# Performance work log

Measured on AMD Instinct MI355X. Metric: run time of the kernel, lower is better.

Reference implementation:

```python
import jax, jax.numpy as jnp
import numpy as np

D_MODEL = 1024
NUM_HEADS = 16
D_K = D_MODEL // NUM_HEADS
MAX_REL = 128


def setup_inputs() -> dict:
    key = jax.random.key(0)
    ks = jax.random.split(key, 16)
    B, S = 4, 2048
    s = 1.0 / np.sqrt(D_MODEL)
    inp = {
        'query': jax.random.normal(ks[0], (B, S, D_MODEL), jnp.float32),
        'key': jax.random.normal(ks[1], (B, S, D_MODEL), jnp.float32),
        'value': jax.random.normal(ks[2], (B, S, D_MODEL), jnp.float32),
        'mask': jax.random.randint(ks[3], (B, 1, 1, S), 0, 2, jnp.int32),
        'Wq': jax.random.normal(ks[4], (D_MODEL, D_MODEL), jnp.float32) * s,
        'bq': jax.random.normal(ks[5], (D_MODEL,), jnp.float32) * 0.02,
        'Wk': jax.random.normal(ks[6], (D_MODEL, D_MODEL), jnp.float32) * s,
        'bk': jax.random.normal(ks[7], (D_MODEL,), jnp.float32) * 0.02,
        'Wv': jax.random.normal(ks[8], (D_MODEL, D_MODEL), jnp.float32) * s,
        'bv': jax.random.normal(ks[9], (D_MODEL,), jnp.float32) * 0.02,
        'Wo': jax.random.normal(ks[10], (D_MODEL, D_MODEL), jnp.float32) * s,
        'bo': jax.random.normal(ks[11], (D_MODEL,), jnp.float32) * 0.02,
        'rel_emb': jax.random.normal(ks[12], (2 * MAX_REL + 1, NUM_HEADS), jnp.float32) * 0.02,
    }
    return inp


def reference(query, key, value, mask, Wq, bq, Wk, bk, Wv, bv, Wo, bo, rel_emb):
    B, S, D = query.shape
    H, dk = NUM_HEADS, D_K
    # Linear projections (torch Linear: x @ W.T + b), split heads -> [B,H,S,dk]
    def proj(x, W, b):
        return (x @ W.T + b).reshape(B, S, H, dk).transpose(0, 2, 1, 3)
    Q = proj(query, Wq, bq)
    K = proj(key, Wk, bk)
    V = proj(value, Wv, bv)
    scores = jnp.einsum('bhqd,bhkd->bhqk', Q, K) / jnp.sqrt(jnp.float32(dk))
    # relative position bias: clamp(j-i, -M, M) + M, gather [S,S,H] -> [H,S,S]
    pos = jnp.arange(S)
    rel = jnp.clip(pos[None, :] - pos[:, None], -MAX_REL, MAX_REL) + MAX_REL
    bias = rel_emb[rel].transpose(2, 0, 1)  # [H,S,S]
    scores = scores + bias[None]
    scores = jnp.where(mask == 0, -jnp.inf, scores)
    weights = jax.nn.softmax(scores, axis=-1)
    weights = jnp.nan_to_num(weights, nan=0.0)  # fully-masked rows -> 0
    # dropout is identity in eval mode
    context = jnp.einsum('bhqk,bhkd->bhqd', weights, V)
    context = context.transpose(0, 2, 1, 3).reshape(B, S, D)
    return context @ Wo.T + bo
```

## Files before the change

### kernel.cpp

```cpp
#include <hip/hip_runtime.h>
#include <cstdint>
#include <cstddef>

typedef __bf16 bf16_t;
typedef __bf16 bf16x8 __attribute__((ext_vector_type(8)));
typedef float f32x4  __attribute__((ext_vector_type(4)));
typedef float f32x16 __attribute__((ext_vector_type(16)));
typedef int   i32x4  __attribute__((ext_vector_type(4)));

#define DEVI static __device__ __forceinline__

DEVI f32x4 mfma16(bf16x8 a, bf16x8 b, f32x4 c) {
  return __builtin_amdgcn_mfma_f32_16x16x32_bf16(a, b, c, 0, 0, 0);
}
DEVI f32x16 mfma32(bf16x8 a, bf16x8 b, f32x16 c) {
  return __builtin_amdgcn_mfma_f32_32x32x16_bf16(a, b, c, 0, 0, 0);
}
DEVI unsigned cvtpk(float lo, float hi) {
  unsigned d;
  asm("v_cvt_pk_bf16_f32 %0, %1, %2" : "=v"(d) : "v"(lo), "v"(hi));
  return d;
}
DEVI void gload_lds16(const bf16_t* g, bf16_t* l) {
  __builtin_amdgcn_global_load_lds(
      (const __attribute__((address_space(1))) void*)g,
      (__attribute__((address_space(3))) void*)l, 16, 0, 0);
}

#define L2E 1.44269504f
#define QSCALE (0.125f * L2E)
#define MASK_NEG (-60000.0f)

__global__ __launch_bounds__(256)
void cvt_f32_bf16(const float* __restrict__ in, bf16_t* __restrict__ out, int n8)
{
  const int i = blockIdx.x * 256 + threadIdx.x;
  if (i >= n8) return;
  float4 a = ((const float4*)in)[2*i];
  float4 b = ((const float4*)in)[2*i + 1];
  bf16x8 o;
  o[0]=(bf16_t)a.x; o[1]=(bf16_t)a.y; o[2]=(bf16_t)a.z; o[3]=(bf16_t)a.w;
  o[4]=(bf16_t)b.x; o[5]=(bf16_t)b.y; o[6]=(bf16_t)b.z; o[7]=(bf16_t)b.w;
  ((bf16x8*)out)[i] = o;
}

__global__ __launch_bounds__(256)
void split_f32_bf16(const float* __restrict__ in, bf16_t* __restrict__ hi,
                    bf16_t* __restrict__ lo, int n8)
{
  const int i = blockIdx.x * 256 + threadIdx.x;
  if (i >= n8) return;
  float4 a = ((const float4*)in)[2*i];
  float4 b = ((const float4*)in)[2*i + 1];
  const float* f = (const float*)&a;
  bf16x8 oh, ol;
  #pragma unroll
  for (int j = 0; j < 4; ++j) { bf16_t h=(bf16_t)f[j]; oh[j]=h; ol[j]=(bf16_t)(f[j]-(float)h); }
  const float* f2 = (const float*)&b;
  #pragma unroll
  for (int j = 0; j < 4; ++j) { bf16_t h=(bf16_t)f2[j]; oh[4+j]=h; ol[4+j]=(bf16_t)(f2[j]-(float)h); }
  ((bf16x8*)hi)[i] = oh;
  ((bf16x8*)lo)[i] = ol;
}

template<int OMODE>
__global__ __launch_bounds__(256)
void proj_gemm97(const bf16_t* __restrict__ A, const bf16_t* __restrict__ W,
                 const float* __restrict__ bias, bf16_t* __restrict__ Out,
                 float oscale)
{
  __shared__ __align__(16) bf16_t As[128 * 64];
  __shared__ __align__(16) bf16_t Bs[128 * 64];
  const int tid  = threadIdx.x;
  const int lane = tid & 63;
  const int w    = tid >> 6;
  const int g = lane >> 4, c = lane & 15;
  const int mq = (w >> 1) * 64, nq = (w & 1) * 64;
  const int bm = blockIdx.y, bn = blockIdx.x;

  const int rsub = lane >> 3;
  const int kc8  = (lane & 7) * 8;

  f32x4 acc[4][4] = {};

  for (int kt = 0; kt < 1024; kt += 64) {
    #pragma unroll
    for (int i = 0; i < 4; ++i) {
      const int inst = w * 4 + i;
      const int row  = inst * 8 + rsub;
      gload_lds16(A + (size_t)(bm*128 + row)*1024 + kt + kc8, &As[inst*512]);
      gload_lds16(W + (size_t)(bn*128 + row)*1024 + kt + kc8, &Bs[inst*512]);
    }
    __syncthreads();
    #pragma unroll
    for (int kk = 0; kk < 64; kk += 32) {
      bf16x8 af[4], bfv[4];
      #pragma unroll
      for (int i = 0; i < 4; ++i) {
        af[i]  = *(const bf16x8*)&As[(mq + i*16 + c)*64 + kk + 8*g];
        bfv[i] = *(const bf16x8*)&Bs[(nq + i*16 + c)*64 + kk + 8*g];
      }
      #pragma unroll
      for (int mi = 0; mi < 4; ++mi)
        #pragma unroll
        for (int ni = 0; ni < 4; ++ni)
          acc[mi][ni] = mfma16(af[mi], bfv[ni], acc[mi][ni]);
    }
    __syncthreads();
  }

  #pragma unroll
  for (int ni = 0; ni < 4; ++ni) {
    const int n = bn*128 + nq + ni*16 + c;
    const float bv = bias[n];
    const int h = n >> 6, d = n & 63;
    #pragma unroll
    for (int mi = 0; mi < 4; ++mi) {
      #pragma unroll
      for (int r = 0; r < 4; ++r) {
        const int m = bm*128 + mq + mi*16 + 4*g + r;
        const float v = (acc[mi][ni][r] + bv) * oscale;
        const int bb = m >> 11, s = m & 2047;
        if (OMODE == 1)
          Out[(((size_t)(bb*16 + h))*2048 + s)*64 + d] = (bf16_t)v;
        else
          Out[(((size_t)(bb*16 + h))*64 + d)*2048 + s] = (bf16_t)v;
      }
    }
  }
}

__global__ __launch_bounds__(256)
void out_gemm97(const bf16_t* __restrict__ Ahg, const bf16_t* __restrict__ Alg,
                const bf16_t* __restrict__ Bhg, const bf16_t* __restrict__ Blg,
                const float* __restrict__ bias, float* __restrict__ Out)
{
  __shared__ __align__(16) bf16_t Ahs[128 * 64];
  __shared__ __align__(16) bf16_t Als[128 * 64];
  __shared__ __align__(16) bf16_t Bhs[128 * 64];
  __shared__ __align__(16) bf16_t Bls[128 * 64];
  const int tid  = threadIdx.x;
  const int lane = tid & 63;
  const int w    = tid >> 6;
  const int g = lane >> 4, c = lane & 15;
  const int mq = (w >> 1) * 64, nq = (w & 1) * 64;
  const int bm = blockIdx.y, bn = blockIdx.x;

  const int rsub = lane >> 3;
  const int kc8  = (lane & 7) * 8;

  f32x4 acc[4][4] = {};

  for (int kt = 0; kt < 1024; kt += 64) {
    #pragma unroll
    for (int i = 0; i < 4; ++i) {
      const int inst = w * 4 + i;
      const int row  = inst * 8 + rsub;
      const size_t ga = (size_t)(bm*128 + row)*1024 + kt + kc8;
      const size_t gb = (size_t)(bn*128 + row)*1024 + kt + kc8;
      gload_lds16(Ahg + ga, &Ahs[inst*512]);
      gload_lds16(Alg + ga, &Als[inst*512]);
      gload_lds16(Bhg + gb, &Bhs[inst*512]);
      gload_lds16(Blg + gb, &Bls[inst*512]);
    }
    __syncthreads();
    #pragma unroll
    for (int kk = 0; kk < 64; kk += 32) {
      bf16x8 afh[4], afl[4], bfh[4], bfl[4];
      #pragma unroll
      for (int i = 0; i < 4; ++i) {
        const int ar = (mq + i*16 + c)*64 + kk + 8*g;
        const int br = (nq + i*16 + c)*64 + kk + 8*g;
        afh[i] = *(const bf16x8*)&Ahs[ar];
        afl[i] = *(const bf16x8*)&Als[ar];
        bfh[i] = *(const bf16x8*)&Bhs[br];
        bfl[i] = *(const bf16x8*)&Bls[br];
      }
      #pragma unroll
      for (int mi = 0; mi < 4; ++mi)
        #pragma unroll
        for (int ni = 0; ni < 4; ++ni) {
          acc[mi][ni] = mfma16(afh[mi], bfh[ni], acc[mi][ni]);
          acc[mi][ni] = mfma16(afl[mi], bfh[ni], acc[mi][ni]);
          acc[mi][ni] = mfma16(afh[mi], bfl[ni], acc[mi][ni]);
        }
    }
    __syncthreads();
  }

  #pragma unroll
  for (int ni = 0; ni < 4; ++ni) {
    const int n = bn*128 + nq + ni*16 + c;
    const float bv = bias[n];
    #pragma unroll
    for (int mi = 0; mi < 4; ++mi)
      #pragma unroll
      for (int r = 0; r < 4; ++r) {
        const int m = bm*128 + mq + mi*16 + 4*g + r;
        Out[(size_t)m*1024 + n] = acc[mi][ni][r] + bv;
      }
  }
}

__global__ __launch_bounds__(256)
void attn_kernel(const bf16_t* __restrict__ Q, const bf16_t* __restrict__ K,
                 const bf16_t* __restrict__ Vt, const int* __restrict__ mask,
                 const float* __restrict__ rel_emb,
                 bf16_t* __restrict__ Ch, bf16_t* __restrict__ Cl)
{
  __shared__ float relc[257];
  __shared__ float maskadd[2048];
  __shared__ float linv[4][32];
  __shared__ __align__(16) bf16_t Ks[2][64][72];
  __shared__ __align__(16) bf16_t Vs[2][64][72];

  const int tid  = threadIdx.x;
  const int w    = tid >> 6;
  const int lane = tid & 63;
  const int lq   = lane & 31;
  const int hi   = lane >> 5;

  const int bid = blockIdx.x;
  const int n   = (bid & 7) * 128 + (bid >> 3);
  const int bh  = n >> 4;
  const int qblk= n & 15;
  const int b = bh >> 4, h = bh & 15;
  const int qw = qblk * 128 + w * 32;

  const bf16_t* Qb = Q  + ((size_t)bh * 2048) * 64;
  const bf16_t* Kb = K  + ((size_t)bh * 2048) * 64;
  const bf16_t* Vb = Vt + ((size_t)bh * 64) * 2048;

  const int sr  = tid >> 2;
  const int soff= (tid & 3) * 16;

  for (int i = tid; i < 257; i += 256)  relc[i] = rel_emb[i * 16 + h] * L2E;
  for (int i = tid; i < 2048; i += 256) maskadd[i] = mask[b * 2048 + i] ? 0.0f : MASK_NEG;

  {
    const bf16_t* kp = Kb + (size_t)sr * 64 + soff;
    const bf16_t* vp = Vb + (size_t)sr * 2048 + soff;
    i32x4 k0 = *(const i32x4*)kp, k1 = *(const i32x4*)(kp + 8);
    i32x4 v0 = *(const i32x4*)vp, v1 = *(const i32x4*)(vp + 8);
    *(i32x4*)&Ks[0][sr][soff] = k0;  *(i32x4*)&Ks[0][sr][soff + 8] = k1;
    *(i32x4*)&Vs[0][sr][soff] = v0;  *(i32x4*)&Vs[0][sr][soff + 8] = v1;
  }
  __syncthreads();

  bf16x8 qf[4];
  #pragma unroll
  for (int dc = 0; dc < 4; ++dc)
    qf[dc] = *(const bf16x8*)&Qb[(size_t)(qw + lq) * 64 + dc * 16 + 8 * hi];

  const float biasLo = relc[0];
  const float biasHi = relc[256];

  f32x16 O0 = {}, O1 = {};
  float lsum = 0.0f;

  auto SOFTMAX = [&](const f32x16& sa, int kvc, float* p) {
    const int d0 = kvc - qw;
    if (d0 >= 160 || d0 <= -160) {
      const float cb = (d0 >= 160) ? biasHi : biasLo;
      #pragma unroll
      for (int reg = 0; reg < 16; ++reg) {
        const int krow = (reg & 3) + 8 * (reg >> 2) + 4 * hi;
        p[reg] = exp2f(sa[reg] + (cb + maskadd[kvc + krow]));
      }
    } else {
      #pragma unroll
      for (int reg = 0; reg < 16; ++reg) {
        const int krow = (reg & 3) + 8 * (reg >> 2) + 4 * hi;
        int rr = kvc + krow - (qw + lq);
        rr = rr < -128 ? -128 : (rr > 128 ? 128 : rr);
        p[reg] = exp2f(sa[reg] + relc[rr + 128] + maskadd[kvc + krow]);
      }
    }
    #pragma unroll
    for (int reg = 0; reg < 16; ++reg) lsum += p[reg];
  };

  auto PACK = [&](const float* p, bf16x8& pa0, bf16x8& pa1) {
    unsigned w0 = cvtpk(p[0], p[1]), w1 = cvtpk(p[2], p[3]);
    unsigned w2 = cvtpk(p[4], p[5]), w3 = cvtpk(p[6], p[7]);
    asm volatile("v_permlane32_swap_b32 %0, %1" : "+v"(w0), "+v"(w2));
    asm volatile("v_permlane32_swap_b32 %0, %1" : "+v"(w1), "+v"(w3));
    i32x4 pw0 = { (int)w0, (int)w1, (int)w2, (int)w3 };
    pa0 = __builtin_bit_cast(bf16x8, pw0);
    unsigned w4 = cvtpk(p[8],  p[9]),  w5 = cvtpk(p[10], p[11]);
    unsigned w6 = cvtpk(p[12], p[13]), w7 = cvtpk(p[14], p[15]);
    asm volatile("v_permlane32_swap_b32 %0, %1" : "+v"(w4), "+v"(w6));
    asm volatile("v_permlane32_swap_b32 %0, %1" : "+v"(w5), "+v"(w7));
    i32x4 pw1 = { (int)w4, (int)w5, (int)w6, (int)w7 };
    pa1 = __builtin_bit_cast(bf16x8, pw1);
  };

  for (int t = 0; t < 32; ++t) {
    const int kv  = t * 64;
    const int cur = t & 1, nxt = cur ^ 1;
    const bool more = (t + 1 < 32);

    i32x4 k0, k1, v0, v1;
    if (more) {
      const bf16_t* kp = Kb + (size_t)(kv + 64 + sr) * 64 + soff;
      const bf16_t* vp = Vb + (size_t)sr * 2048 + (kv + 64) + soff;
      k0 = *(const i32x4*)kp;  k1 = *(const i32x4*)(kp + 8);
      v0 = *(const i32x4*)vp;  v1 = *(const i32x4*)(vp + 8);
    }

    bf16x8 kf0[4], kf1[4];
    #pragma unroll
    for (int dc = 0; dc < 4; ++dc)
      kf0[dc] = *(const bf16x8*)&Ks[cur][lq][dc * 16 + 8 * hi];
    #pragma unroll
    for (int dc = 0; dc < 4; ++dc)
      kf1[dc] = *(const bf16x8*)&Ks[cur][32 + lq][dc * 16 + 8 * hi];

    f32x16 sa0 = {}, sa1 = {};
    __builtin_amdgcn_s_setprio(1);
    #pragma unroll
    for (int dc = 0; dc < 4; ++dc) sa0 = mfma32(kf0[dc], qf[dc], sa0);
    #pragma unroll
    for (int dc = 0; dc < 4; ++dc) sa1 = mfma32(kf1[dc], qf[dc], sa1);
    __builtin_amdgcn_s_setprio(0);

    bf16x8 vf[4][2];
    #pragma unroll
    for (int kcg = 0; kcg < 4; ++kcg)
      #pragma unroll
      for (int db = 0; db < 2; ++db)
        vf[kcg][db] = *(const bf16x8*)&Vs[cur][db * 32 + lq][kcg * 16 + 8 * hi];

    float p[16];
    bf16x8 pa0, pa1;
    SOFTMAX(sa0, kv, p);
    PACK(p, pa0, pa1);
    __builtin_amdgcn_s_setprio(1);
    O0 = mfma32(pa0, vf[0][0], O0);
    O1 = mfma32(pa0, vf[0][1], O1);
    O0 = mfma32(pa1, vf[1][0], O0);
    O1 = mfma32(pa1, vf[1][1], O1);
    __builtin_amdgcn_s_setprio(0);

    SOFTMAX(sa1, kv + 32, p);
    PACK(p, pa0, pa1);
    __builtin_amdgcn_s_setprio(1);
    O0 = mfma32(pa0, vf[2][0], O0);
    O1 = mfma32(pa0, vf[2][1], O1);
    O0 = mfma32(pa1, vf[3][0], O0);
    O1 = mfma32(pa1, vf[3][1], O1);
    __builtin_amdgcn_s_setprio(0);

    if (more) {
      *(i32x4*)&Ks[nxt][sr][soff] = k0;  *(i32x4*)&Ks[nxt][sr][soff + 8] = k1;
      *(i32x4*)&Vs[nxt][sr][soff] = v0;  *(i32x4*)&Vs[nxt][sr][soff + 8] = v1;
    }
    __syncthreads();
  }

  lsum += __shfl_xor(lsum, 32);
  if (lane < 32) linv[w][lane] = (lsum > 0.0f) ? 1.0f / lsum : 0.0f;
  asm volatile("s_waitcnt lgkmcnt(0)" ::: "memory");
  __builtin_amdgcn_sched_barrier(0);

  #pragma unroll
  for (int reg = 0; reg < 16; ++reg) {
    const int qrow = (reg & 3) + 8 * (reg >> 2) + 4 * hi;
    const float iv = linv[w][qrow];
    const int s = qw + qrow;
    const size_t base = ((size_t)(b * 2048 + s)) * 1024 + h * 64 + lq;
    const float o0 = O0[reg] * iv, o1 = O1[reg] * iv;
    const bf16_t h0 = (bf16_t)o0, h1 = (bf16_t)o1;
    Ch[base]      = h0;  Cl[base]      = (bf16_t)(o0 - (float)h0);
    Ch[base + 32] = h1;  Cl[base + 32] = (bf16_t)(o1 - (float)h1);
  }
}

extern "C" void kernel_launch(void* const* d_in, const int* in_sizes, int n_in,
                              void* d_out, int out_size, void* d_ws, size_t ws_size,
                              hipStream_t stream)
{
  const float* q    = (const float*)d_in[0];
  const float* k    = (const float*)d_in[1];
  const float* v    = (const float*)d_in[2];
  const int*   mask = (const int*)  d_in[3];
  const float* Wq   = (const float*)d_in[4];
  const float* bq   = (const float*)d_in[5];
  const float* Wk   = (const float*)d_in[6];
  const float* bk   = (const float*)d_in[7];
  const float* Wv   = (const float*)d_in[8];
  const float* bv   = (const float*)d_in[9];
  const float* Wo   = (const float*)d_in[10];
  const float* bo   = (const float*)d_in[11];
  const float* rel  = (const float*)d_in[12];

  char* wsb = (char*)d_ws;
  bf16_t* Qw  = (bf16_t*)(wsb);
  bf16_t* Kw  = (bf16_t*)(wsb + ((size_t) 16 << 20));
  bf16_t* Vw  = (bf16_t*)(wsb + ((size_t) 32 << 20));
  bf16_t* Qc  = (bf16_t*)(wsb + ((size_t) 48 << 20));
  bf16_t* Kc  = (bf16_t*)(wsb + ((size_t) 64 << 20));
  bf16_t* Vc  = (bf16_t*)(wsb + ((size_t) 80 << 20));
  bf16_t* Wqc = (bf16_t*)(wsb + ((size_t) 96 << 20));
  bf16_t* Wkc = (bf16_t*)(wsb + ((size_t) 98 << 20));
  bf16_t* Wvc = (bf16_t*)(wsb + ((size_t)100 << 20));
  bf16_t* Woh = (bf16_t*)(wsb + ((size_t)102 << 20));
  bf16_t* Wol = (bf16_t*)(wsb + ((size_t)104 << 20));
  bf16_t* Chp = Qc;
  bf16_t* Clp = Kc;

  const int n8t = 8192 * 1024 / 8;
  const int n8w = 1024 * 1024 / 8;
  dim3 bb(256);

  cvt_f32_bf16<<<dim3(4096), bb, 0, stream>>>(q, Qc, n8t);
  cvt_f32_bf16<<<dim3(4096), bb, 0, stream>>>(k, Kc, n8t);
  cvt_f32_bf16<<<dim3(4096), bb, 0, stream>>>(v, Vc, n8t);
  cvt_f32_bf16<<<dim3(512),  bb, 0, stream>>>(Wq, Wqc, n8w);
  cvt_f32_bf16<<<dim3(512),  bb, 0, stream>>>(Wk, Wkc, n8w);
  cvt_f32_bf16<<<dim3(512),  bb, 0, stream>>>(Wv, Wvc, n8w);
  split_f32_bf16<<<dim3(512), bb, 0, stream>>>(Wo, Woh, Wol, n8w);

  dim3 gg(8, 64);
  proj_gemm97<1><<<gg, bb, 0, stream>>>(Qc, Wqc, bq, Qw, QSCALE);
  proj_gemm97<1><<<gg, bb, 0, stream>>>(Kc, Wkc, bk, Kw, 1.0f);
  proj_gemm97<2><<<gg, bb, 0, stream>>>(Vc, Wvc, bv, Vw, 1.0f);
  attn_kernel<<<dim3(1024), bb, 0, stream>>>(Qw, Kw, Vw, mask, rel, Chp, Clp);
  out_gemm97<<<gg, bb, 0, stream>>>(Chp, Clp, Woh, Wol, bo, (float*)d_out);
}
```

Before: 314.0 us.

## Fold key mask into V and compute softmax row sums via extra MFMA

Masked keys now have their V rows zeroed in the V projection epilogue. The softmax denominator is computed by an extra MFMA of P against a bf16 mask-bit vector, instead of adding a -inf-like bias before exp2 and reducing lane sums. This removes per-element mask adds, the scalar lsum reduction and the shared linv buffer. K/V LDS tiles switch from padded rows to XOR-swizzled rows, attn gets a min-occupancy launch bound, and the seven conversion launches are merged into two. The cost is a third accumulator and extra MFMAs per tile. Unmasked exp values of masked keys may overflow without the mask bias, which is a numerical risk.

```diff
diff --git a/kernel.cpp b/kernel.cpp
--- a/kernel.cpp
+++ b/kernel.cpp
@@ -29,13 +29,18 @@
 
 #define L2E 1.44269504f
 #define QSCALE (0.125f * L2E)
-#define MASK_NEG (-60000.0f)
 
 __global__ __launch_bounds__(256)
-void cvt_f32_bf16(const float* __restrict__ in, bf16_t* __restrict__ out, int n8)
+void cvt_qkv(const float* __restrict__ a0, const float* __restrict__ a1,
+             const float* __restrict__ a2, bf16_t* __restrict__ o0,
+             bf16_t* __restrict__ o1, bf16_t* __restrict__ o2, int n8)
 {
   const int i = blockIdx.x * 256 + threadIdx.x;
   if (i >= n8) return;
+  const float* in; bf16_t* out;
+  if (blockIdx.y == 0)      { in = a0; out = o0; }
+  else if (blockIdx.y == 1) { in = a1; out = o1; }
+  else                      { in = a2; out = o2; }
   float4 a = ((const float4*)in)[2*i];
   float4 b = ((const float4*)in)[2*i + 1];
   bf16x8 o;
@@ -45,29 +50,44 @@
 }
 
 __global__ __launch_bounds__(256)
-void split_f32_bf16(const float* __restrict__ in, bf16_t* __restrict__ hi,
-                    bf16_t* __restrict__ lo, int n8)
+void cvt_w(const float* __restrict__ wq, const float* __restrict__ wk,
+           const float* __restrict__ wv, const float* __restrict__ wo,
+           bf16_t* __restrict__ oq, bf16_t* __restrict__ ok,
+           bf16_t* __restrict__ ov, bf16_t* __restrict__ ooh,
+           bf16_t* __restrict__ ool, int n8)
 {
   const int i = blockIdx.x * 256 + threadIdx.x;
   if (i >= n8) return;
-  float4 a = ((const float4*)in)[2*i];
-  float4 b = ((const float4*)in)[2*i + 1];
-  const float* f = (const float*)&a;
-  bf16x8 oh, ol;
-  #pragma unroll
-  for (int j = 0; j < 4; ++j) { bf16_t h=(bf16_t)f[j]; oh[j]=h; ol[j]=(bf16_t)(f[j]-(float)h); }
-  const float* f2 = (const float*)&b;
-  #pragma unroll
-  for (int j = 0; j < 4; ++j) { bf16_t h=(bf16_t)f2[j]; oh[4+j]=h; ol[4+j]=(bf16_t)(f2[j]-(float)h); }
-  ((bf16x8*)hi)[i] = oh;
-  ((bf16x8*)lo)[i] = ol;
+  const int y = blockIdx.y;
+  if (y < 3) {
+    const float* in = (y == 0) ? wq : (y == 1) ? wk : wv;
+    bf16_t* out     = (y == 0) ? oq : (y == 1) ? ok : ov;
+    float4 a = ((const float4*)in)[2*i];
+    float4 b = ((const float4*)in)[2*i + 1];
+    bf16x8 o;
+    o[0]=(bf16_t)a.x; o[1]=(bf16_t)a.y; o[2]=(bf16_t)a.z; o[3]=(bf16_t)a.w;
+    o[4]=(bf16_t)b.x; o[5]=(bf16_t)b.y; o[6]=(bf16_t)b.z; o[7]=(bf16_t)b.w;
+    ((bf16x8*)out)[i] = o;
+  } else {
+    float4 a = ((const float4*)wo)[2*i];
+    float4 b = ((const float4*)wo)[2*i + 1];
+    const float* f = (const float*)&a;
+    bf16x8 oh, ol;
+    #pragma unroll
+    for (int j = 0; j < 4; ++j) { bf16_t h=(bf16_t)f[j]; oh[j]=h; ol[j]=(bf16_t)(f[j]-(float)h); }
+    const float* f2 = (const float*)&b;
+    #pragma unroll
+    for (int j = 0; j < 4; ++j) { bf16_t h=(bf16_t)f2[j]; oh[4+j]=h; ol[4+j]=(bf16_t)(f2[j]-(float)h); }
+    ((bf16x8*)ooh)[i] = oh;
+    ((bf16x8*)ool)[i] = ol;
+  }
 }
 
 template<int OMODE>
 __global__ __launch_bounds__(256)
 void proj_gemm97(const bf16_t* __restrict__ A, const bf16_t* __restrict__ W,
                  const float* __restrict__ bias, bf16_t* __restrict__ Out,
-                 float oscale)
+                 float oscale, const int* __restrict__ mask)
 {
   __shared__ __align__(16) bf16_t As[128 * 64];
   __shared__ __align__(16) bf16_t Bs[128 * 64];
@@ -119,12 +139,14 @@
       #pragma unroll
       for (int r = 0; r < 4; ++r) {
         const int m = bm*128 + mq + mi*16 + 4*g + r;
-        const float v = (acc[mi][ni][r] + bv) * oscale;
         const int bb = m >> 11, s = m & 2047;
-        if (OMODE == 1)
+        float v = (acc[mi][ni][r] + bv) * oscale;
+        if (OMODE == 1) {
           Out[(((size_t)(bb*16 + h))*2048 + s)*64 + d] = (bf16_t)v;
-        else
+        } else {
+          if (mask[bb*2048 + s] == 0) v = 0.0f;
           Out[(((size_t)(bb*16 + h))*64 + d)*2048 + s] = (bf16_t)v;
+        }
       }
     }
   }
@@ -202,17 +224,16 @@
   }
 }
 
-__global__ __launch_bounds__(256)
+__global__ __launch_bounds__(256, 4)
 void attn_kernel(const bf16_t* __restrict__ Q, const bf16_t* __restrict__ K,
                  const bf16_t* __restrict__ Vt, const int* __restrict__ mask,
                  const float* __restrict__ rel_emb,
                  bf16_t* __restrict__ Ch, bf16_t* __restrict__ Cl)
 {
   __shared__ float relc[257];
-  __shared__ float maskadd[2048];
-  __shared__ float linv[4][32];
-  __shared__ __align__(16) bf16_t Ks[2][64][72];
-  __shared__ __align__(16) bf16_t Vs[2][64][72];
+  __shared__ bf16_t maskbit[2048];
+  __shared__ __align__(16) bf16_t Ks[2][64 * 64];
+  __shared__ __align__(16) bf16_t Vs[2][64 * 64];
 
   const int tid  = threadIdx.x;
   const int w    = tid >> 6;
@@ -232,18 +253,20 @@
   const bf16_t* Vb = Vt + ((size_t)bh * 64) * 2048;
 
   const int sr  = tid >> 2;
-  const int soff= (tid & 3) * 16;
+  const int so  = (tid & 3) * 16;
+  const int sx0 = so ^ ((sr & 7) << 3);
+  const int sx1 = (so + 8) ^ ((sr & 7) << 3);
 
   for (int i = tid; i < 257; i += 256)  relc[i] = rel_emb[i * 16 + h] * L2E;
-  for (int i = tid; i < 2048; i += 256) maskadd[i] = mask[b * 2048 + i] ? 0.0f : MASK_NEG;
+  for (int i = tid; i < 2048; i += 256) maskbit[i] = mask[b * 2048 + i] ? (bf16_t)1.0f : (bf16_t)0.0f;
 
   {
-    const bf16_t* kp = Kb + (size_t)sr * 64 + soff;
-    const bf16_t* vp = Vb + (size_t)sr * 2048 + soff;
+    const bf16_t* kp = Kb + (size_t)sr * 64 + so;
+    const bf16_t* vp = Vb + (size_t)sr * 2048 + so;
     i32x4 k0 = *(const i32x4*)kp, k1 = *(const i32x4*)(kp + 8);
     i32x4 v0 = *(const i32x4*)vp, v1 = *(const i32x4*)(vp + 8);
-    *(i32x4*)&Ks[0][sr][soff] = k0;  *(i32x4*)&Ks[0][sr][soff + 8] = k1;
-    *(i32x4*)&Vs[0][sr][soff] = v0;  *(i32x4*)&Vs[0][sr][soff + 8] = v1;
+    *(i32x4*)&Ks[0][sr*64 + sx0] = k0;  *(i32x4*)&Ks[0][sr*64 + sx1] = k1;
+    *(i32x4*)&Vs[0][sr*64 + sx0] = v0;  *(i32x4*)&Vs[0][sr*64 + sx1] = v1;
   }
   __syncthreads();
 
@@ -255,29 +278,24 @@
   const float biasLo = relc[0];
   const float biasHi = relc[256];
 
-  f32x16 O0 = {}, O1 = {};
-  float lsum = 0.0f;
+  f32x16 O0 = {}, O1 = {}, Ol = {};
 
   auto SOFTMAX = [&](const f32x16& sa, int kvc, float* p) {
     const int d0 = kvc - qw;
     if (d0 >= 160 || d0 <= -160) {
       const float cb = (d0 >= 160) ? biasHi : biasLo;
       #pragma unroll
-      for (int reg = 0; reg < 16; ++reg) {
-        const int krow = (reg & 3) + 8 * (reg >> 2) + 4 * hi;
-        p[reg] = exp2f(sa[reg] + (cb + maskadd[kvc + krow]));
-      }
+      for (int reg = 0; reg < 16; ++reg)
+        p[reg] = exp2f(sa[reg] + cb);
     } else {
       #pragma unroll
       for (int reg = 0; reg < 16; ++reg) {
         const int krow = (reg & 3) + 8 * (reg >> 2) + 4 * hi;
         int rr = kvc + krow - (qw + lq);
         rr = rr < -128 ? -128 : (rr > 128 ? 128 : rr);
-        p[reg] = exp2f(sa[reg] + relc[rr + 128] + maskadd[kvc + krow]);
+        p[reg] = exp2f(sa[reg] + relc[rr + 128]);
       }
     }
-    #pragma unroll
-    for (int reg = 0; reg < 16; ++reg) lsum += p[reg];
   };
 
   auto PACK = [&](const float* p, bf16x8& pa0, bf16x8& pa1) {
@@ -302,19 +320,19 @@
 
     i32x4 k0, k1, v0, v1;
     if (more) {
-      const bf16_t* kp = Kb + (size_t)(kv + 64 + sr) * 64 + soff;
-      const bf16_t* vp = Vb + (size_t)sr * 2048 + (kv + 64) + soff;
+      const bf16_t* kp = Kb + (size_t)(kv + 64 + sr) * 64 + so;
+      const bf16_t* vp = Vb + (size_t)sr * 2048 + (kv + 64) + so;
       k0 = *(const i32x4*)kp;  k1 = *(const i32x4*)(kp + 8);
       v0 = *(const i32x4*)vp;  v1 = *(const i32x4*)(vp + 8);
     }
 
     bf16x8 kf0[4], kf1[4];
     #pragma unroll
-    for (int dc = 0; dc < 4; ++dc)
-      kf0[dc] = *(const bf16x8*)&Ks[cur][lq][dc * 16 + 8 * hi];
-    #pragma unroll
-    for (int dc = 0; dc < 4; ++dc)
-      kf1[dc] = *(const bf16x8*)&Ks[cur][32 + lq][dc * 16 + 8 * hi];
+    for (int dc = 0; dc < 4; ++dc) {
+      const int col = (dc * 16 + 8 * hi);
+      kf0[dc] = *(const bf16x8*)&Ks[cur][lq*64        + (col ^ ((lq & 7) << 3))];
+      kf1[dc] = *(const bf16x8*)&Ks[cur][(32+lq)*64   + (col ^ ((lq & 7) << 3))];
+    }
 
     f32x16 sa0 = {}, sa1 = {};
     __builtin_amdgcn_s_setprio(1);
@@ -323,50 +341,63 @@
     #pragma unroll
     for (int dc = 0; dc < 4; ++dc) sa1 = mfma32(kf1[dc], qf[dc], sa1);
     __builtin_amdgcn_s_setprio(0);
-
-    bf16x8 vf[4][2];
-    #pragma unroll
-    for (int kcg = 0; kcg < 4; ++kcg)
-      #pragma unroll
-      for (int db = 0; db < 2; ++db)
-        vf[kcg][db] = *(const bf16x8*)&Vs[cur][db * 32 + lq][kcg * 16 + 8 * hi];
 
     float p[16];
     bf16x8 pa0, pa1;
     SOFTMAX(sa0, kv, p);
     PACK(p, pa0, pa1);
-    __builtin_amdgcn_s_setprio(1);
-    O0 = mfma32(pa0, vf[0][0], O0);
-    O1 = mfma32(pa0, vf[0][1], O1);
-    O0 = mfma32(pa1, vf[1][0], O0);
-    O1 = mfma32(pa1, vf[1][1], O1);
-    __builtin_amdgcn_s_setprio(0);
+    {
+      bf16x8 vf00, vf01, vf10, vf11;
+      const int c0 = (0 * 16 + 8 * hi), c1 = (1 * 16 + 8 * hi);
+      vf00 = *(const bf16x8*)&Vs[cur][lq*64      + (c0 ^ ((lq & 7) << 3))];
+      vf01 = *(const bf16x8*)&Vs[cur][(32+lq)*64 + (c0 ^ ((lq & 7) << 3))];
+      vf10 = *(const bf16x8*)&Vs[cur][lq*64      + (c1 ^ ((lq & 7) << 3))];
+      vf11 = *(const bf16x8*)&Vs[cur][(32+lq)*64 + (c1 ^ ((lq & 7) << 3))];
+      bf16x8 mbA = *(const bf16x8*)&maskbit[kv + 8 * hi];
+      bf16x8 mbB = *(const bf16x8*)&maskbit[kv + 16 + 8 * hi];
+      __builtin_amdgcn_s_setprio(1);
+      O0 = mfma32(pa0, vf00, O0);
+      O1 = mfma32(pa0, vf01, O1);
+      Ol = mfma32(pa0, mbA,  Ol);
+      O0 = mfma32(pa1, vf10, O0);
+      O1 = mfma32(pa1, vf11, O1);
+      Ol = mfma32(pa1, mbB,  Ol);
+      __builtin_amdgcn_s_setprio(0);
+    }
 
     SOFTMAX(sa1, kv + 32, p);
     PACK(p, pa0, pa1);
-    __builtin_amdgcn_s_setprio(1);
-    O0 = mfma32(pa0, vf[2][0], O0);
-    O1 = mfma32(pa0, vf[2][1], O1);
-    O0 = mfma32(pa1, vf[3][0], O0);
-    O1 = mfma32(pa1, vf[3][1], O1);
-    __builtin_amdgcn_s_setprio(0);
+    {
+      bf16x8 vf00, vf01, vf10, vf11;
+      const int c0 = (2 * 16 + 8 * hi), c1 = (3 * 16 + 8 * hi);
+      vf00 = *(const bf16x8*)&Vs[cur][lq*64      + (c0 ^ ((lq & 7) << 3))];
+      vf01 = *(const bf16x8*)&Vs[cur][(32+lq)*64 + (c0 ^ ((lq & 7) << 3))];
+      vf10 = *(const bf16x8*)&Vs[cur][lq*64      + (c1 ^ ((lq & 7) << 3))];
+      vf11 = *(const bf16x8*)&Vs[cur][(32+lq)*64 + (c1 ^ ((lq & 7) << 3))];
+      bf16x8 mbA = *(const bf16x8*)&maskbit[kv + 32 + 8 * hi];
+      bf16x8 mbB = *(const bf16x8*)&maskbit[kv + 48 + 8 * hi];
+      __builtin_amdgcn_s_setprio(1);
+      O0 = mfma32(pa0, vf00, O0);
+      O1 = mfma32(pa0, vf01, O1);
+      Ol = mfma32(pa0, mbA,  Ol);
+      O0 = mfma32(pa1, vf10, O0);
+      O1 = mfma32(pa1, vf11, O1);
+      Ol = mfma32(pa1, mbB,  Ol);
+      __builtin_amdgcn_s_setprio(0);
+    }
 
     if (more) {
-      *(i32x4*)&Ks[nxt][sr][soff] = k0;  *(i32x4*)&Ks[nxt][sr][soff + 8] = k1;
-      *(i32x4*)&Vs[nxt][sr][soff] = v0;  *(i32x4*)&Vs[nxt][sr][soff + 8] = v1;
+      *(i32x4*)&Ks[nxt][sr*64 + sx0] = k0;  *(i32x4*)&Ks[nxt][sr*64 + sx1] = k1;
+      *(i32x4*)&Vs[nxt][sr*64 + sx0] = v0;  *(i32x4*)&Vs[nxt][sr*64 + sx1] = v1;
     }
     __syncthreads();
   }
-
-  lsum += __shfl_xor(lsum, 32);
-  if (lane < 32) linv[w][lane] = (lsum > 0.0f) ? 1.0f / lsum : 0.0f;
-  asm volatile("s_waitcnt lgkmcnt(0)" ::: "memory");
-  __builtin_amdgcn_sched_barrier(0);
 
   #pragma unroll
   for (int reg = 0; reg < 16; ++reg) {
     const int qrow = (reg & 3) + 8 * (reg >> 2) + 4 * hi;
-    const float iv = linv[w][qrow];
+    const float sum = Ol[reg];
+    const float iv = (sum > 0.0f) ? 1.0f / sum : 0.0f;
     const int s = qw + qrow;
     const size_t base = ((size_t)(b * 2048 + s)) * 1024 + h * 64 + lq;
     const float o0 = O0[reg] * iv, o1 = O1[reg] * iv;
@@ -413,18 +444,13 @@
   const int n8w = 1024 * 1024 / 8;
   dim3 bb(256);
 
-  cvt_f32_bf16<<<dim3(4096), bb, 0, stream>>>(q, Qc, n8t);
-  cvt_f32_bf16<<<dim3(4096), bb, 0, stream>>>(k, Kc, n8t);
-  cvt_f32_bf16<<<dim3(4096), bb, 0, stream>>>(v, Vc, n8t);
-  cvt_f32_bf16<<<dim3(512),  bb, 0, stream>>>(Wq, Wqc, n8w);
-  cvt_f32_bf16<<<dim3(512),  bb, 0, stream>>>(Wk, Wkc, n8w);
-  cvt_f32_bf16<<<dim3(512),  bb, 0, stream>>>(Wv, Wvc, n8w);
-  split_f32_bf16<<<dim3(512), bb, 0, stream>>>(Wo, Woh, Wol, n8w);
+  cvt_qkv<<<dim3(4096, 3), bb, 0, stream>>>(q, k, v, Qc, Kc, Vc, n8t);
+  cvt_w<<<dim3(512, 4), bb, 0, stream>>>(Wq, Wk, Wv, Wo, Wqc, Wkc, Wvc, Woh, Wol, n8w);
 
   dim3 gg(8, 64);
-  proj_gemm97<1><<<gg, bb, 0, stream>>>(Qc, Wqc, bq, Qw, QSCALE);
-  proj_gemm97<1><<<gg, bb, 0, stream>>>(Kc, Wkc, bk, Kw, 1.0f);
-  proj_gemm97<2><<<gg, bb, 0, stream>>>(Vc, Wvc, bv, Vw, 1.0f);
+  proj_gemm97<1><<<gg, bb, 0, stream>>>(Qc, Wqc, bq, Qw, QSCALE, mask);
+  proj_gemm97<1><<<gg, bb, 0, stream>>>(Kc, Wkc, bk, Kw, 1.0f, mask);
+  proj_gemm97<2><<<gg, bb, 0, stream>>>(Vc, Wvc, bv, Vw, 1.0f, mask);
   attn_kernel<<<dim3(1024), bb, 0, stream>>>(Qw, Kw, Vw, mask, rel, Chp, Clp);
   out_gemm97<<<gg, bb, 0, stream>>>(Chp, Clp, Woh, Wol, bo, (float*)d_out);
 }
```

Result: slower. 412.7 us (+31.4%).
